# Performance work log

Hardware: AMD Instinct MI355X
Metric: run time of the kernel (lower is better)

## Reference

```python
import jax, jax.numpy as jnp
import numpy as np

N_NODES = 100_000
N_EDGES = 1_250_000
IN_FEATS, N_HIDDEN, N_CLASSES = 64, 64, 32


def setup_inputs() -> dict:
    key = jax.random.key(0)
    ks = jax.random.split(key, 8)
    x = jax.random.normal(ks[0], (N_NODES, IN_FEATS), dtype=jnp.float32)
    src = jax.random.randint(ks[1], (N_EDGES,), 0, N_NODES, dtype=jnp.int64)
    dst = jax.random.randint(ks[2], (N_EDGES,), 0, N_NODES, dtype=jnp.int64)
    s1 = 1.0 / np.sqrt(IN_FEATS)
    s2 = 1.0 / np.sqrt(N_HIDDEN)
    W_self1 = jax.random.normal(ks[3], (IN_FEATS, N_HIDDEN), dtype=jnp.float32) * s1
    W_neigh1 = jax.random.normal(ks[4], (IN_FEATS, N_HIDDEN), dtype=jnp.float32) * s1
    b1 = jnp.zeros((N_HIDDEN,), dtype=jnp.float32)
    W_self2 = jax.random.normal(ks[5], (N_HIDDEN, N_CLASSES), dtype=jnp.float32) * s2
    W_neigh2 = jax.random.normal(ks[6], (N_HIDDEN, N_CLASSES), dtype=jnp.float32) * s2
    b2 = jnp.zeros((N_CLASSES,), dtype=jnp.float32)
    return dict(x=x, src=src, dst=dst, W_self1=W_self1, W_neigh1=W_neigh1, b1=b1,
                W_self2=W_self2, W_neigh2=W_neigh2, b2=b2)


def _sage_conv(h, src, dst, W_self, W_neigh, b):
    # mean aggregation over in-neighbors: gather src feats, segment-sum by dst
    n = h.shape[0]
    msg = h[src]  # [E, d] -- dominant memory traffic
    agg = jax.ops.segment_sum(msg, dst, num_segments=n)
    deg = jax.ops.segment_sum(jnp.ones_like(dst, dtype=h.dtype), dst, num_segments=n)
    h_neigh = agg / jnp.maximum(deg, 1.0)[:, None]  # zero-degree nodes get 0 (DGL behavior)
    return h @ W_self + h_neigh @ W_neigh + b


def reference(x, src, dst, W_self1, W_neigh1, b1, W_self2, W_neigh2, b2):
    h = _sage_conv(x, src, dst, W_self1, W_neigh1, b1)
    h = jax.nn.relu(h)
    # dropout(p=0.5) is identity in eval mode
    return _sage_conv(h, src, dst, W_self2, W_neigh2, b2)
```

## Files before the change

### kernel.cpp

```cpp
#include <hip/hip_runtime.h>
#include <hip/hip_bf16.h>


#define NF 64
#define BW 256
#define BSH 8
#define MAXB 512
#define CAPMAX 8192
#define P1_CHUNK 2048
#define H1S 68

typedef __attribute__((ext_vector_type(8))) short short8;
typedef __attribute__((ext_vector_type(8))) unsigned short ushort8v;
typedef __attribute__((ext_vector_type(4))) float floatx4;

__device__ __forceinline__ short bf16hi(float v) {
    __hip_bfloat16 h = __float2bfloat16(v);
    return *(short*)&h;
}
__device__ __forceinline__ float bf2f(short s) {
    __hip_bfloat16 h = *(__hip_bfloat16*)&s;
    return __bfloat162float(h);
}
__device__ __forceinline__ float bits2f(unsigned short u) {
    unsigned int x = ((unsigned int)u) << 16;
    union { unsigned int i; float f; } c; c.i = x; return c.f;
}


__global__ __launch_bounds__(512) void zero_kernel(int* __restrict__ g) {
    if (threadIdx.x < MAXB) g[threadIdx.x] = 0;
}


__global__ __launch_bounds__(256) void p1_dense1_kernel(
        const int* __restrict__ src, const int* __restrict__ dst,
        int* __restrict__ gcursor, unsigned* __restrict__ bucket,
        int E, int nbuckets, int dblocks,
        const float* __restrict__ X,
        const float* __restrict__ Wself,
        const float* __restrict__ Wneigh,
        const float* __restrict__ bias,
        float* __restrict__ outA,
        unsigned short* __restrict__ outB,
        int N,
        const float* __restrict__ Ws2,
        const float* __restrict__ Wn2,
        unsigned short* __restrict__ w2p,
        int wpackBlk) {
    __shared__ int smem_i[9216];
    const int tid = threadIdx.x;

    if ((int)blockIdx.x == wpackBlk) {
        for (int i = tid; i < 64 * 64; i += 256) {
            int n = i & 63, k = i >> 6;
            float v = (n < 32) ? Ws2[k * 32 + n] : Wn2[k * 32 + (n - 32)];
            short hv = bf16hi(v);
            w2p[n * 64 + k] = (unsigned short)hv;
            w2p[4096 + n * 64 + k] = (unsigned short)bf16hi(v - bf2f(hv));
        }
        return;
    }

    if ((int)blockIdx.x >= dblocks) {
        int* cnt   = smem_i;
        int* cbase = smem_i + MAXB;
        const int bid = blockIdx.x - dblocks;
        const int beg = bid * P1_CHUNK;
        const int end = min(E, beg + P1_CHUNK);
        for (int i = tid; i < nbuckets; i += 256) cnt[i] = 0;
        __syncthreads();
        for (int e = beg + tid; e < end; e += 256)
            atomicAdd(&cnt[dst[e] >> BSH], 1);
        __syncthreads();
        for (int i = tid; i < nbuckets; i += 256) {
            int c = cnt[i];
            cbase[i] = c ? atomicAdd(&gcursor[i], c) : 0;
            cnt[i] = 0;
        }
        __syncthreads();
        for (int e = beg + tid; e < end; e += 256) {
            int d = dst[e];
            int r = d >> BSH;
            int p = cbase[r] + atomicAdd(&cnt[r], 1);
            if (p < CAPMAX)
                bucket[(size_t)r * CAPMAX + p] = ((unsigned)src[e] << BSH) | (unsigned)(d & (BW - 1));
        }
        return;
    }

    constexpr int NT = 8, NSELF = 4, NO = 128, HALF = 64;
    unsigned short* wh = (unsigned short*)smem_i;
    unsigned short* wl = wh + NO * 72;
    for (int i = tid; i < NO * 64; i += 256) {
        int n = i & (NO - 1), k = i / NO;
        float v = (n < HALF) ? Wself[k * HALF + n] : Wneigh[k * HALF + (n - HALF)];
        short hv = bf16hi(v);
        wh[n * 72 + k] = (unsigned short)hv;
        wl[n * 72 + k] = (unsigned short)bf16hi(v - bf2f(hv));
    }

    const int lane = tid & 63;
    const int wid  = tid >> 6;
    const int m = lane & 15, quad = lane >> 4;
    const int rowblk = blockIdx.x * 128 + wid * 32;

    floatx4 acc[2][NT];
    #pragma unroll
    for (int rt = 0; rt < 2; ++rt)
        #pragma unroll
        for (int t = 0; t < NT; ++t) acc[rt][t] = (floatx4)(0.f);

    short8 ah[2][2], al[2][2];
    #pragma unroll
    for (int rt = 0; rt < 2; ++rt) {
        int r = rowblk + rt * 16 + m;
        if (r >= N) r = N - 1;
        const float* xp = X + (size_t)r * 64 + quad * 8;
        #pragma unroll
        for (int h = 0; h < 2; ++h) {
            floatx4 f0 = *(const floatx4*)(xp + h * 32);
            floatx4 f1 = *(const floatx4*)(xp + h * 32 + 4);
            short8 hi, lo;
            #pragma unroll
            for (int j = 0; j < 4; ++j) {
                short hv = bf16hi(f0[j]);
                hi[j] = hv; lo[j] = bf16hi(f0[j] - bf2f(hv));
                short hv2 = bf16hi(f1[j]);
                hi[4 + j] = hv2; lo[4 + j] = bf16hi(f1[j] - bf2f(hv2));
            }
            ah[rt][h] = hi; al[rt][h] = lo;
        }
    }
    __syncthreads();

    #pragma unroll
    for (int t = 0; t < NT; ++t) {
        int n = t * 16 + m;
        const unsigned short* ph = wh + n * 72 + quad * 8;
        const unsigned short* pl = wl + n * 72 + quad * 8;
        #pragma unroll
        for (int h = 0; h < 2; ++h) {
            short8 bh = *(const short8*)(ph + h * 32);
            short8 bl = *(const short8*)(pl + h * 32);
            #pragma unroll
            for (int rt = 0; rt < 2; ++rt) {
                acc[rt][t] = __builtin_amdgcn_mfma_f32_16x16x32_bf16(ah[rt][h], bh, acc[rt][t], 0, 0, 0);
                acc[rt][t] = __builtin_amdgcn_mfma_f32_16x16x32_bf16(al[rt][h], bh, acc[rt][t], 0, 0, 0);
                acc[rt][t] = __builtin_amdgcn_mfma_f32_16x16x32_bf16(ah[rt][h], bl, acc[rt][t], 0, 0, 0);
            }
        }
    }

    #pragma unroll
    for (int rt = 0; rt < 2; ++rt) {
        #pragma unroll
        for (int t = 0; t < NT; ++t) {
            #pragma unroll
            for (int r4 = 0; r4 < 4; ++r4) {
                int row = rowblk + rt * 16 + quad * 4 + r4;
                if (row < N) {
                    if (t < NSELF) {
                        int col = t * 16 + m;
                        outA[(size_t)row * 64 + col] = acc[rt][t][r4] + bias[col];
                    } else {
                        int col = (t - NSELF) * 16 + m;
                        outB[(size_t)row * 64 + col] = (unsigned short)bf16hi(acc[rt][t][r4]);
                    }
                }
            }
        }
    }
}


__global__ __launch_bounds__(256) void p2_csr_kernel(const unsigned* __restrict__ bucket,
                                                     const int* __restrict__ gcursor,
                                                     int* __restrict__ row_start,
                                                     int* __restrict__ csr_src,
                                                     int N, int nbuckets) {
    __shared__ unsigned stage[CAPMAX];
    __shared__ int cnt[BW];
    __shared__ int excl[BW];
    const int r = blockIdx.x;
    const int tid = threadIdx.x;

    int partial = 0;
    for (int i = tid; i < r; i += 256) partial += min(gcursor[i], CAPMAX);
    excl[tid] = partial;
    __syncthreads();
    for (int off = 128; off > 0; off >>= 1) {
        if (tid < off) excl[tid] += excl[tid + off];
        __syncthreads();
    }
    const int base = excl[0];
    const int sz = min(gcursor[r], CAPMAX);
    const unsigned* bsrc = bucket + (size_t)r * CAPMAX;
    __syncthreads();

    cnt[tid] = 0;
    __syncthreads();
    for (int i = tid; i < sz; i += 256) {
        unsigned v = bsrc[i];
        stage[i] = v;
        atomicAdd(&cnt[v & (BW - 1)], 1);
    }
    __syncthreads();
    excl[tid] = cnt[tid];
    __syncthreads();
    for (int off = 1; off < BW; off <<= 1) {
        int v0 = (tid >= off) ? excl[tid - off] : 0;
        __syncthreads();
        excl[tid] += v0;
        __syncthreads();
    }
    int node = r * BW + tid;
    if (node < N) row_start[node] = base + excl[tid] - cnt[tid];
    if (r == nbuckets - 1 && tid == 0) row_start[N] = base + sz;
    __syncthreads();
    cnt[tid] = excl[tid] - cnt[tid];
    __syncthreads();
    for (int i = tid; i < sz; i += 256) {
        unsigned v = stage[i];
        int p = atomicAdd(&cnt[v & (BW - 1)], 1);
        csr_src[base + p] = (int)(v >> BSH);
    }
}


__global__ __launch_bounds__(256) void agg64_d2_kernel(
        const unsigned short* __restrict__ t1n,
        const float* __restrict__ xs,
        const int* __restrict__ row_start,
        const int* __restrict__ csr_src,
        const unsigned short* __restrict__ w2p,
        const float* __restrict__ b2,
        float* __restrict__ outD,
        unsigned short* __restrict__ t2n,
        int N) {
    __shared__ float h1s[16][H1S];
    const int tid = threadIdx.x;

    const int lane = tid & 63;
    const int wid  = tid >> 6;
    const int half = lane >> 5;
    const int g = (lane >> 3) & 3;
    const int c = lane & 7;
    const int nbase = blockIdx.x * 16;

    const int m = lane & 15, quad = lane >> 4;
    const int coln = wid * 16 + m;
    const unsigned short* pb = w2p + coln * 64 + quad * 8;
    short8 bhf[2], blf[2];
    #pragma unroll
    for (int h = 0; h < 2; ++h) {
        bhf[h] = *(const short8*)(pb + h * 32);
        blf[h] = *(const short8*)(pb + h * 32 + 4096);
    }

    #pragma unroll
    for (int q = 0; q < 2; ++q) {
        const int ln = wid * 4 + q * 2 + half;
        const int n = nbase + ln;
        float acc[8] = {0.f, 0.f, 0.f, 0.f, 0.f, 0.f, 0.f, 0.f};
        int beg = 0, end = 0;
        if (n < N) { beg = row_start[n]; end = row_start[n + 1]; }
        for (int j = beg + g; j < end; j += 8) {
            int j2 = j + 4;
            int s0 = csr_src[j];
            ushort8v u0 = *(const ushort8v*)(t1n + (size_t)s0 * 64 + c * 8);
            if (j2 < end) {
                int s1 = csr_src[j2];
                ushort8v u1 = *(const ushort8v*)(t1n + (size_t)s1 * 64 + c * 8);
                #pragma unroll
                for (int i = 0; i < 8; ++i) acc[i] += bits2f(u0[i]) + bits2f(u1[i]);
            } else {
                #pragma unroll
                for (int i = 0; i < 8; ++i) acc[i] += bits2f(u0[i]);
            }
        }
        #pragma unroll
        for (int i = 0; i < 8; ++i) {
            float v = acc[i];
            v += __shfl_xor(v, 8);
            v += __shfl_xor(v, 16);
            acc[i] = v;
        }
        if (g == 0) {
            floatx4 h0, h1v;
            if (n < N) {
                float invd = 1.0f / fmaxf((float)(end - beg), 1.0f);
                size_t o = (size_t)n * 64 + c * 8;
                floatx4 x0 = *(const floatx4*)(xs + o);
                floatx4 x1 = *(const floatx4*)(xs + o + 4);
                #pragma unroll
                for (int i = 0; i < 4; ++i) {
                    h0[i]  = fmaxf(x0[i] + acc[i] * invd, 0.f);
                    h1v[i] = fmaxf(x1[i] + acc[4 + i] * invd, 0.f);
                }
            } else {
                h0 = (floatx4)(0.f); h1v = (floatx4)(0.f);
            }
            *(floatx4*)&h1s[ln][c * 8]     = h0;
            *(floatx4*)&h1s[ln][c * 8 + 4] = h1v;
        }
    }
    __syncthreads();

    short8 ah[2], al[2];
    #pragma unroll
    for (int h = 0; h < 2; ++h) {
        const float* hp = &h1s[m][quad * 8 + h * 32];
        floatx4 f0 = *(const floatx4*)hp;
        floatx4 f1 = *(const floatx4*)(hp + 4);
        short8 hi, lo;
        #pragma unroll
        for (int j = 0; j < 4; ++j) {
            short hv = bf16hi(f0[j]);
            hi[j] = hv; lo[j] = bf16hi(f0[j] - bf2f(hv));
            short hv2 = bf16hi(f1[j]);
            hi[4 + j] = hv2; lo[4 + j] = bf16hi(f1[j] - bf2f(hv2));
        }
        ah[h] = hi; al[h] = lo;
    }
    floatx4 acc2 = (floatx4)(0.f);
    #pragma unroll
    for (int h = 0; h < 2; ++h) {
        acc2 = __builtin_amdgcn_mfma_f32_16x16x32_bf16(ah[h], bhf[h], acc2, 0, 0, 0);
        acc2 = __builtin_amdgcn_mfma_f32_16x16x32_bf16(al[h], bhf[h], acc2, 0, 0, 0);
        acc2 = __builtin_amdgcn_mfma_f32_16x16x32_bf16(ah[h], blf[h], acc2, 0, 0, 0);
    }
    #pragma unroll
    for (int r4 = 0; r4 < 4; ++r4) {
        int node = nbase + quad * 4 + r4;
        if (node < N) {
            if (coln < 32) outD[(size_t)node * 32 + coln] = acc2[r4] + b2[coln];
            else t2n[(size_t)node * 32 + (coln - 32)] = (unsigned short)bf16hi(acc2[r4]);
        }
    }
}


__global__ __launch_bounds__(256) void agg32_kernel(float* io,
                                                    const unsigned short* __restrict__ t2n,
                                                    const int* __restrict__ row_start,
                                                    const int* __restrict__ csr_src, int N) {
    int n = (blockIdx.x * blockDim.x + threadIdx.x) >> 6;
    if (n >= N) return;
    int lane = threadIdx.x & 63;
    int g = lane >> 2, c = lane & 3;
    int beg = row_start[n], end = row_start[n + 1];
    float acc[8] = {0.f, 0.f, 0.f, 0.f, 0.f, 0.f, 0.f, 0.f};
    for (int j = beg + g; j < end; j += 32) {
        int j2 = j + 16;
        int s0 = csr_src[j];
        ushort8v u0 = *(const ushort8v*)(t2n + (size_t)s0 * 32 + c * 8);
        if (j2 < end) {
            int s1 = csr_src[j2];
            ushort8v u1 = *(const ushort8v*)(t2n + (size_t)s1 * 32 + c * 8);
            #pragma unroll
            for (int i = 0; i < 8; ++i) acc[i] += bits2f(u0[i]) + bits2f(u1[i]);
        } else {
            #pragma unroll
            for (int i = 0; i < 8; ++i) acc[i] += bits2f(u0[i]);
        }
    }
    #pragma unroll
    for (int i = 0; i < 8; ++i) {
        float v = acc[i];
        v += __shfl_xor(v, 4);
        v += __shfl_xor(v, 8);
        v += __shfl_xor(v, 16);
        v += __shfl_xor(v, 32);
        acc[i] = v;
    }
    if (g == 0) {
        float inv = 1.0f / fmaxf((float)(end - beg), 1.0f);
        size_t o = (size_t)n * 32 + c * 8;
        floatx4 s0 = *(const floatx4*)(io + o);
        floatx4 s1 = *(const floatx4*)(io + o + 4);
        floatx4 r0, r1;
        #pragma unroll
        for (int i = 0; i < 4; ++i) {
            r0[i] = s0[i] + acc[i] * inv;
            r1[i] = s1[i] + acc[4 + i] * inv;
        }
        *(floatx4*)(io + o) = r0;
        *(floatx4*)(io + o + 4) = r1;
    }
}


__global__ __launch_bounds__(256) void deg_kernel(const int* __restrict__ dst,
                                                  float* __restrict__ deg, int E) {
    int e = blockIdx.x * blockDim.x + threadIdx.x;
    if (e < E) atomicAdd(&deg[dst[e]], 1.0f);
}

__global__ __launch_bounds__(256) void agg_atomic_kernel(const float* __restrict__ feats,
                                                         const int* __restrict__ src,
                                                         const int* __restrict__ dst,
                                                         float* __restrict__ agg, int E) {
    int tid = blockIdx.x * blockDim.x + threadIdx.x;
    if (tid >= E * NF) return;
    int e = tid >> 6, f = tid & 63;
    atomicAdd(&agg[(size_t)dst[e] * NF + f], feats[(size_t)src[e] * NF + f]);
}

__global__ __launch_bounds__(256) void layer1_fb_kernel(const float* __restrict__ x,
                                                        const float* __restrict__ agg,
                                                        const float* __restrict__ deg,
                                                        const float* __restrict__ Wself,
                                                        const float* __restrict__ Wneigh,
                                                        const float* __restrict__ b,
                                                        float* __restrict__ h1, int N) {
    int tid = blockIdx.x * blockDim.x + threadIdx.x;
    if (tid >= N * NF) return;
    int n = tid >> 6, c = tid & 63;
    float inv = 1.0f / fmaxf(deg[n], 1.0f);
    const float* xrow = x + (size_t)n * NF;
    const float* arow = agg + (size_t)n * NF;
    float acc = b[c];
    #pragma unroll
    for (int k = 0; k < NF; ++k) {
        acc += xrow[k] * Wself[k * NF + c];
        acc += (arow[k] * inv) * Wneigh[k * NF + c];
    }
    h1[tid] = fmaxf(acc, 0.f);
}

__global__ __launch_bounds__(256) void layer2_fb_kernel(const float* __restrict__ h1,
                                                        const float* __restrict__ agg,
                                                        const float* __restrict__ deg,
                                                        const float* __restrict__ Wself,
                                                        const float* __restrict__ Wneigh,
                                                        const float* __restrict__ b,
                                                        float* __restrict__ out, int N) {
    int tid = blockIdx.x * blockDim.x + threadIdx.x;
    if (tid >= N * 32) return;
    int n = tid >> 5, c = tid & 31;
    float inv = 1.0f / fmaxf(deg[n], 1.0f);
    const float* hrow = h1 + (size_t)n * NF;
    const float* arow = agg + (size_t)n * NF;
    float acc = b[c];
    #pragma unroll
    for (int k = 0; k < NF; ++k) {
        acc += hrow[k] * Wself[k * 32 + c];
        acc += (arow[k] * inv) * Wneigh[k * 32 + c];
    }
    out[tid] = acc;
}


extern "C" void kernel_launch(void* const* d_in, const int* in_sizes, int n_in,
                              void* d_out, int out_size, void* d_ws, size_t ws_size,
                              hipStream_t stream) {
    const float* x        = (const float*)d_in[0];
    const int*   src      = (const int*)d_in[1];
    const int*   dst      = (const int*)d_in[2];
    const float* W_self1  = (const float*)d_in[3];
    const float* W_neigh1 = (const float*)d_in[4];
    const float* b1       = (const float*)d_in[5];
    const float* W_self2  = (const float*)d_in[6];
    const float* W_neigh2 = (const float*)d_in[7];
    const float* b2       = (const float*)d_in[8];
    float* out = (float*)d_out;

    const int N = in_sizes[0] / NF;
    const int E = in_sizes[1];
    const int nbuckets = (N + BW - 1) / BW;

    const size_t rsPad = ((size_t)N + 8) & ~7ull;
    int* gcursor   = (int*)d_ws;
    unsigned short* w2p = (unsigned short*)(gcursor + MAXB);
    int* row_start = (int*)(w2p + 8192);
    int* csr_src   = row_start + rsPad;
    uintptr_t pa = (uintptr_t)(csr_src + (((size_t)E + 7) & ~7ull));
    pa = (pa + 127) & ~(uintptr_t)127;
    float* bufA = (float*)pa;
    unsigned* bucket = (unsigned*)bufA;
    unsigned short* t1n = (unsigned short*)(bufA + (size_t)N * NF);
    unsigned short* t2n = t1n + (size_t)N * NF;
    size_t need = (size_t)((char*)(t2n + (size_t)N * 32) - (char*)d_ws);

    bool fast = ws_size >= need
             && nbuckets <= MAXB
             && (size_t)nbuckets * CAPMAX <= (size_t)N * NF
             && (size_t)E * 2 / (size_t)nbuckets <= CAPMAX
             && N < (1 << 24)
             && out_size >= N * 32;

    if (fast) {
        zero_kernel<<<1, 512, 0, stream>>>(gcursor);
        int dblocks  = (N + 127) / 128;
        int p1blocks = (E + P1_CHUNK - 1) / P1_CHUNK;
        unsigned* bucket2 = (unsigned*)(t2n + (((size_t)N * 32 + 63) & ~63ull));
        size_t need2 = (size_t)((char*)(bucket2 + (size_t)nbuckets * CAPMAX) - (char*)d_ws);
        if (ws_size >= need2) {
            p1_dense1_kernel<<<dblocks + p1blocks + 1, 256, 0, stream>>>(
                src, dst, gcursor, bucket2, E, nbuckets, dblocks,
                x, W_self1, W_neigh1, b1, bufA, t1n, N,
                W_self2, W_neigh2, w2p, dblocks + p1blocks);
            p2_csr_kernel<<<nbuckets, 256, 0, stream>>>(bucket2, gcursor,
                                                        row_start, csr_src, N, nbuckets);
        } else {
            p1_dense1_kernel<<<p1blocks + 1, 256, 0, stream>>>(
                src, dst, gcursor, bucket, E, nbuckets, 0,
                x, W_self1, W_neigh1, b1, bufA, t1n, N,
                W_self2, W_neigh2, w2p, p1blocks);
            p2_csr_kernel<<<nbuckets, 256, 0, stream>>>(bucket, gcursor,
                                                        row_start, csr_src, N, nbuckets);
            p1_dense1_kernel<<<dblocks, 256, 0, stream>>>(
                src, dst, gcursor, bucket, E, nbuckets, dblocks,
                x, W_self1, W_neigh1, b1, bufA, t1n, N,
                W_self2, W_neigh2, w2p, -1);
        }
        agg64_d2_kernel<<<(N + 15) / 16, 256, 0, stream>>>(
            t1n, bufA, row_start, csr_src, w2p, b2, out, t2n, N);
        agg32_kernel<<<(N * 64 + 255) / 256, 256, 0, stream>>>(out, t2n,
                                                               row_start, csr_src, N);
    } else {
        float* deg = (float*)d_ws;
        float* agg = deg + N;
        float* h1  = agg + (size_t)N * NF;
        hipMemsetAsync(deg, 0, (size_t)(N + (size_t)N * NF) * sizeof(float), stream);
        deg_kernel<<<(E + 255) / 256, 256, 0, stream>>>(dst, deg, E);
        int at = E * NF;
        agg_atomic_kernel<<<(at + 255) / 256, 256, 0, stream>>>(x, src, dst, agg, E);
        layer1_fb_kernel<<<(N * NF + 255) / 256, 256, 0, stream>>>(x, agg, deg, W_self1,
                                                                   W_neigh1, b1, h1, N);
        hipMemsetAsync(agg, 0, (size_t)N * NF * sizeof(float), stream);
        agg_atomic_kernel<<<(at + 255) / 256, 256, 0, stream>>>(h1, src, dst, agg, E);
        layer2_fb_kernel<<<(N * 32 + 255) / 256, 256, 0, stream>>>(h1, agg, deg, W_self2,
                                                                   W_neigh2, b2, out, N);
    }
}
```

Baseline: 216.7 us.

## Prepack layer weights in a prep kernel and interleave two-node gathers in aggregation

Layer-1 and layer-2 weights are now split into hi/lo bf16 and packed once by a small prep kernel that also zeroes the cursors. The dense layer-1 blocks read the packed weights from global memory, so each block no longer repacks them into 36KB of LDS and waits on a barrier, which should also raise occupancy. The layer-2 aggregation walks both of a wave's nodes in one loop with four independent gathers in flight, using clamped indices and predicated adds. The self-feature loads are issued before the reduction to hide their latency. The cost is extra wasted loads when the two nodes differ in degree, and one more small launch.

```diff
diff --git a/kernel.cpp b/kernel.cpp
--- a/kernel.cpp
+++ b/kernel.cpp
@@ -28,8 +28,31 @@
 }
 
 
-__global__ __launch_bounds__(512) void zero_kernel(int* __restrict__ g) {
-    if (threadIdx.x < MAXB) g[threadIdx.x] = 0;
+__global__ __launch_bounds__(256) void prep_kernel(
+        int* __restrict__ gcursor,
+        const float* __restrict__ Ws1, const float* __restrict__ Wn1,
+        const float* __restrict__ Ws2, const float* __restrict__ Wn2,
+        unsigned short* __restrict__ w1p, unsigned short* __restrict__ w2p) {
+    const int tid = threadIdx.x;
+    if (blockIdx.x == 0) {
+        for (int i = tid; i < MAXB; i += 256) gcursor[i] = 0;
+        return;
+    }
+    const int part = blockIdx.x - 1;
+    for (int i = tid; i < 32 * 64; i += 256) {
+        int n = part * 32 + (i >> 6), k = i & 63;
+        float v = (n < 64) ? Ws1[k * 64 + n] : Wn1[k * 64 + (n - 64)];
+        short hv = bf16hi(v);
+        w1p[n * 64 + k] = (unsigned short)hv;
+        w1p[8192 + n * 64 + k] = (unsigned short)bf16hi(v - bf2f(hv));
+    }
+    for (int i = tid; i < 16 * 64; i += 256) {
+        int n = part * 16 + (i >> 6), k = i & 63;
+        float v = (n < 32) ? Ws2[k * 32 + n] : Wn2[k * 32 + (n - 32)];
+        short hv = bf16hi(v);
+        w2p[n * 64 + k] = (unsigned short)hv;
+        w2p[4096 + n * 64 + k] = (unsigned short)bf16hi(v - bf2f(hv));
+    }
 }
 
 
@@ -38,29 +61,13 @@
         int* __restrict__ gcursor, unsigned* __restrict__ bucket,
         int E, int nbuckets, int dblocks,
         const float* __restrict__ X,
-        const float* __restrict__ Wself,
-        const float* __restrict__ Wneigh,
+        const unsigned short* __restrict__ w1p,
         const float* __restrict__ bias,
         float* __restrict__ outA,
         unsigned short* __restrict__ outB,
-        int N,
-        const float* __restrict__ Ws2,
-        const float* __restrict__ Wn2,
-        unsigned short* __restrict__ w2p,
-        int wpackBlk) {
-    __shared__ int smem_i[9216];
+        int N) {
+    __shared__ int smem_i[2 * MAXB];
     const int tid = threadIdx.x;
-
-    if ((int)blockIdx.x == wpackBlk) {
-        for (int i = tid; i < 64 * 64; i += 256) {
-            int n = i & 63, k = i >> 6;
-            float v = (n < 32) ? Ws2[k * 32 + n] : Wn2[k * 32 + (n - 32)];
-            short hv = bf16hi(v);
-            w2p[n * 64 + k] = (unsigned short)hv;
-            w2p[4096 + n * 64 + k] = (unsigned short)bf16hi(v - bf2f(hv));
-        }
-        return;
-    }
 
     if ((int)blockIdx.x >= dblocks) {
         int* cnt   = smem_i;
@@ -89,17 +96,7 @@
         return;
     }
 
-    constexpr int NT = 8, NSELF = 4, NO = 128, HALF = 64;
-    unsigned short* wh = (unsigned short*)smem_i;
-    unsigned short* wl = wh + NO * 72;
-    for (int i = tid; i < NO * 64; i += 256) {
-        int n = i & (NO - 1), k = i / NO;
-        float v = (n < HALF) ? Wself[k * HALF + n] : Wneigh[k * HALF + (n - HALF)];
-        short hv = bf16hi(v);
-        wh[n * 72 + k] = (unsigned short)hv;
-        wl[n * 72 + k] = (unsigned short)bf16hi(v - bf2f(hv));
-    }
-
+    constexpr int NT = 8, NSELF = 4;
     const int lane = tid & 63;
     const int wid  = tid >> 6;
     const int m = lane & 15, quad = lane >> 4;
@@ -132,13 +129,12 @@
             ah[rt][h] = hi; al[rt][h] = lo;
         }
     }
-    __syncthreads();
 
     #pragma unroll
     for (int t = 0; t < NT; ++t) {
         int n = t * 16 + m;
-        const unsigned short* ph = wh + n * 72 + quad * 8;
-        const unsigned short* pl = wl + n * 72 + quad * 8;
+        const unsigned short* ph = w1p + n * 64 + quad * 8;
+        const unsigned short* pl = ph + 8192;
         #pragma unroll
         for (int h = 0; h < 2; ++h) {
             short8 bh = *(const short8*)(ph + h * 32);
@@ -237,10 +233,9 @@
         const float* __restrict__ b2,
         float* __restrict__ outD,
         unsigned short* __restrict__ t2n,
-        int N) {
+        int N, int E) {
     __shared__ float h1s[16][H1S];
     const int tid = threadIdx.x;
-
     const int lane = tid & 63;
     const int wid  = tid >> 6;
     const int half = lane >> 5;
@@ -248,62 +243,94 @@
     const int c = lane & 7;
     const int nbase = blockIdx.x * 16;
 
+    const int ln0 = wid * 4 + half;
+    const int ln1 = ln0 + 2;
+    const int n0 = nbase + ln0, n1 = nbase + ln1;
+    int beg0 = 0, end0 = 0, beg1 = 0, end1 = 0;
+    if (n0 < N) { beg0 = row_start[n0]; end0 = row_start[n0 + 1]; }
+    if (n1 < N) { beg1 = row_start[n1]; end1 = row_start[n1 + 1]; }
+
+    float a0[8] = {0.f, 0.f, 0.f, 0.f, 0.f, 0.f, 0.f, 0.f};
+    float a1[8] = {0.f, 0.f, 0.f, 0.f, 0.f, 0.f, 0.f, 0.f};
+    int j0 = beg0 + g, j1 = beg1 + g;
+    const int Em1 = E - 1;
+    while ((j0 < end0) || (j1 < end1)) {
+        int s0 = csr_src[min(j0, Em1)];
+        int s1 = csr_src[min(j0 + 4, Em1)];
+        int s2 = csr_src[min(j1, Em1)];
+        int s3 = csr_src[min(j1 + 4, Em1)];
+        s0 = ((unsigned)s0 < (unsigned)N) ? s0 : 0;
+        s1 = ((unsigned)s1 < (unsigned)N) ? s1 : 0;
+        s2 = ((unsigned)s2 < (unsigned)N) ? s2 : 0;
+        s3 = ((unsigned)s3 < (unsigned)N) ? s3 : 0;
+        ushort8v u0 = *(const ushort8v*)(t1n + (size_t)s0 * 64 + c * 8);
+        ushort8v u1 = *(const ushort8v*)(t1n + (size_t)s1 * 64 + c * 8);
+        ushort8v u2 = *(const ushort8v*)(t1n + (size_t)s2 * 64 + c * 8);
+        ushort8v u3 = *(const ushort8v*)(t1n + (size_t)s3 * 64 + c * 8);
+        const bool c00 = j0 < end0, c01 = j0 + 4 < end0;
+        const bool c10 = j1 < end1, c11 = j1 + 4 < end1;
+        #pragma unroll
+        for (int i = 0; i < 8; ++i) {
+            a0[i] += (c00 ? bits2f(u0[i]) : 0.f) + (c01 ? bits2f(u1[i]) : 0.f);
+            a1[i] += (c10 ? bits2f(u2[i]) : 0.f) + (c11 ? bits2f(u3[i]) : 0.f);
+        }
+        j0 += 8; j1 += 8;
+    }
+
     const int m = lane & 15, quad = lane >> 4;
     const int coln = wid * 16 + m;
     const unsigned short* pb = w2p + coln * 64 + quad * 8;
-    short8 bhf[2], blf[2];
-    #pragma unroll
-    for (int h = 0; h < 2; ++h) {
-        bhf[h] = *(const short8*)(pb + h * 32);
-        blf[h] = *(const short8*)(pb + h * 32 + 4096);
-    }
-
-    #pragma unroll
-    for (int q = 0; q < 2; ++q) {
-        const int ln = wid * 4 + q * 2 + half;
-        const int n = nbase + ln;
-        float acc[8] = {0.f, 0.f, 0.f, 0.f, 0.f, 0.f, 0.f, 0.f};
-        int beg = 0, end = 0;
-        if (n < N) { beg = row_start[n]; end = row_start[n + 1]; }
-        for (int j = beg + g; j < end; j += 8) {
-            int j2 = j + 4;
-            int s0 = csr_src[j];
-            ushort8v u0 = *(const ushort8v*)(t1n + (size_t)s0 * 64 + c * 8);
-            if (j2 < end) {
-                int s1 = csr_src[j2];
-                ushort8v u1 = *(const ushort8v*)(t1n + (size_t)s1 * 64 + c * 8);
-                #pragma unroll
-                for (int i = 0; i < 8; ++i) acc[i] += bits2f(u0[i]) + bits2f(u1[i]);
-            } else {
-                #pragma unroll
-                for (int i = 0; i < 8; ++i) acc[i] += bits2f(u0[i]);
+    short8 bhf0 = *(const short8*)(pb);
+    short8 bhf1 = *(const short8*)(pb + 32);
+    short8 blf0 = *(const short8*)(pb + 4096);
+    short8 blf1 = *(const short8*)(pb + 4096 + 32);
+
+    floatx4 x00 = (floatx4)(0.f), x01 = (floatx4)(0.f);
+    floatx4 x10 = (floatx4)(0.f), x11 = (floatx4)(0.f);
+    if (g == 0) {
+        if (n0 < N) {
+            const float* p = xs + (size_t)n0 * 64 + c * 8;
+            x00 = *(const floatx4*)p; x01 = *(const floatx4*)(p + 4);
+        }
+        if (n1 < N) {
+            const float* p = xs + (size_t)n1 * 64 + c * 8;
+            x10 = *(const floatx4*)p; x11 = *(const floatx4*)(p + 4);
+        }
+    }
+
+    #pragma unroll
+    for (int i = 0; i < 8; ++i) {
+        float v = a0[i];
+        v += __shfl_xor(v, 8);
+        v += __shfl_xor(v, 16);
+        a0[i] = v;
+        float w = a1[i];
+        w += __shfl_xor(w, 8);
+        w += __shfl_xor(w, 16);
+        a1[i] = w;
+    }
+    if (g == 0) {
+        floatx4 h0, h1v;
+        if (n0 < N) {
+            float invd = 1.0f / fmaxf((float)(end0 - beg0), 1.0f);
+            #pragma unroll
+            for (int i = 0; i < 4; ++i) {
+                h0[i]  = fmaxf(x00[i] + a0[i] * invd, 0.f);
+                h1v[i] = fmaxf(x01[i] + a0[4 + i] * invd, 0.f);
             }
-        }
-        #pragma unroll
-        for (int i = 0; i < 8; ++i) {
-            float v = acc[i];
-            v += __shfl_xor(v, 8);
-            v += __shfl_xor(v, 16);
-            acc[i] = v;
-        }
-        if (g == 0) {
-            floatx4 h0, h1v;
-            if (n < N) {
-                float invd = 1.0f / fmaxf((float)(end - beg), 1.0f);
-                size_t o = (size_t)n * 64 + c * 8;
-                floatx4 x0 = *(const floatx4*)(xs + o);
-                floatx4 x1 = *(const floatx4*)(xs + o + 4);
-                #pragma unroll
-                for (int i = 0; i < 4; ++i) {
-                    h0[i]  = fmaxf(x0[i] + acc[i] * invd, 0.f);
-                    h1v[i] = fmaxf(x1[i] + acc[4 + i] * invd, 0.f);
-                }
-            } else {
-                h0 = (floatx4)(0.f); h1v = (floatx4)(0.f);
+        } else { h0 = (floatx4)(0.f); h1v = (floatx4)(0.f); }
+        *(floatx4*)&h1s[ln0][c * 8]     = h0;
+        *(floatx4*)&h1s[ln0][c * 8 + 4] = h1v;
+        if (n1 < N) {
+            float invd = 1.0f / fmaxf((float)(end1 - beg1), 1.0f);
+            #pragma unroll
+            for (int i = 0; i < 4; ++i) {
+                h0[i]  = fmaxf(x10[i] + a1[i] * invd, 0.f);
+                h1v[i] = fmaxf(x11[i] + a1[4 + i] * invd, 0.f);
             }
-            *(floatx4*)&h1s[ln][c * 8]     = h0;
-            *(floatx4*)&h1s[ln][c * 8 + 4] = h1v;
-        }
+        } else { h0 = (floatx4)(0.f); h1v = (floatx4)(0.f); }
+        *(floatx4*)&h1s[ln1][c * 8]     = h0;
+        *(floatx4*)&h1s[ln1][c * 8 + 4] = h1v;
     }
     __syncthreads();
 
@@ -324,12 +351,12 @@
         ah[h] = hi; al[h] = lo;
     }
     floatx4 acc2 = (floatx4)(0.f);
-    #pragma unroll
-    for (int h = 0; h < 2; ++h) {
-        acc2 = __builtin_amdgcn_mfma_f32_16x16x32_bf16(ah[h], bhf[h], acc2, 0, 0, 0);
-        acc2 = __builtin_amdgcn_mfma_f32_16x16x32_bf16(al[h], bhf[h], acc2, 0, 0, 0);
-        acc2 = __builtin_amdgcn_mfma_f32_16x16x32_bf16(ah[h], blf[h], acc2, 0, 0, 0);
-    }
+    acc2 = __builtin_amdgcn_mfma_f32_16x16x32_bf16(ah[0], bhf0, acc2, 0, 0, 0);
+    acc2 = __builtin_amdgcn_mfma_f32_16x16x32_bf16(al[0], bhf0, acc2, 0, 0, 0);
+    acc2 = __builtin_amdgcn_mfma_f32_16x16x32_bf16(ah[0], blf0, acc2, 0, 0, 0);
+    acc2 = __builtin_amdgcn_mfma_f32_16x16x32_bf16(ah[1], bhf1, acc2, 0, 0, 0);
+    acc2 = __builtin_amdgcn_mfma_f32_16x16x32_bf16(al[1], bhf1, acc2, 0, 0, 0);
+    acc2 = __builtin_amdgcn_mfma_f32_16x16x32_bf16(ah[1], blf1, acc2, 0, 0, 0);
     #pragma unroll
     for (int r4 = 0; r4 < 4; ++r4) {
         int node = nbase + quad * 4 + r4;
@@ -350,6 +377,12 @@
     int lane = threadIdx.x & 63;
     int g = lane >> 2, c = lane & 3;
     int beg = row_start[n], end = row_start[n + 1];
+    floatx4 s0v = (floatx4)(0.f), s1v = (floatx4)(0.f);
+    size_t o = (size_t)n * 32 + c * 8;
+    if (g == 0) {
+        s0v = *(const floatx4*)(io + o);
+        s1v = *(const floatx4*)(io + o + 4);
+    }
     float acc[8] = {0.f, 0.f, 0.f, 0.f, 0.f, 0.f, 0.f, 0.f};
     for (int j = beg + g; j < end; j += 32) {
         int j2 = j + 16;
@@ -376,14 +409,11 @@
     }
     if (g == 0) {
         float inv = 1.0f / fmaxf((float)(end - beg), 1.0f);
-        size_t o = (size_t)n * 32 + c * 8;
-        floatx4 s0 = *(const floatx4*)(io + o);
-        floatx4 s1 = *(const floatx4*)(io + o + 4);
         floatx4 r0, r1;
         #pragma unroll
         for (int i = 0; i < 4; ++i) {
-            r0[i] = s0[i] + acc[i] * inv;
-            r1[i] = s1[i] + acc[4 + i] * inv;
+            r0[i] = s0v[i] + acc[i] * inv;
+            r1[i] = s1v[i] + acc[4 + i] * inv;
         }
         *(floatx4*)(io + o) = r0;
         *(floatx4*)(io + o + 4) = r1;
@@ -473,7 +503,8 @@
     const size_t rsPad = ((size_t)N + 8) & ~7ull;
     int* gcursor   = (int*)d_ws;
     unsigned short* w2p = (unsigned short*)(gcursor + MAXB);
-    int* row_start = (int*)(w2p + 8192);
+    unsigned short* w1p = w2p + 8192;
+    int* row_start = (int*)(w1p + 16384);
     int* csr_src   = row_start + rsPad;
     uintptr_t pa = (uintptr_t)(csr_src + (((size_t)E + 7) & ~7ull));
     pa = (pa + 127) & ~(uintptr_t)127;
@@ -491,32 +522,30 @@
              && out_size >= N * 32;
 
     if (fast) {
-        zero_kernel<<<1, 512, 0, stream>>>(gcursor);
+        prep_kernel<<<5, 256, 0, stream>>>(gcursor, W_self1, W_neigh1,
+                                           W_self2, W_neigh2, w1p, w2p);
         int dblocks  = (N + 127) / 128;
         int p1blocks = (E + P1_CHUNK - 1) / P1_CHUNK;
         unsigned* bucket2 = (unsigned*)(t2n + (((size_t)N * 32 + 63) & ~63ull));
         size_t need2 = (size_t)((char*)(bucket2 + (size_t)nbuckets * CAPMAX) - (char*)d_ws);
         if (ws_size >= need2) {
-            p1_dense1_kernel<<<dblocks + p1blocks + 1, 256, 0, stream>>>(
+            p1_dense1_kernel<<<dblocks + p1blocks, 256, 0, stream>>>(
                 src, dst, gcursor, bucket2, E, nbuckets, dblocks,
-                x, W_self1, W_neigh1, b1, bufA, t1n, N,
-                W_self2, W_neigh2, w2p, dblocks + p1blocks);
+                x, w1p, b1, bufA, t1n, N);
             p2_csr_kernel<<<nbuckets, 256, 0, stream>>>(bucket2, gcursor,
                                                         row_start, csr_src, N, nbuckets);
         } else {
-            p1_dense1_kernel<<<p1blocks + 1, 256, 0, stream>>>(
+            p1_dense1_kernel<<<p1blocks, 256, 0, stream>>>(
                 src, dst, gcursor, bucket, E, nbuckets, 0,
-                x, W_self1, W_neigh1, b1, bufA, t1n, N,
-                W_self2, W_neigh2, w2p, p1blocks);
+                x, w1p, b1, bufA, t1n, N);
             p2_csr_kernel<<<nbuckets, 256, 0, stream>>>(bucket, gcursor,
                                                         row_start, csr_src, N, nbuckets);
             p1_dense1_kernel<<<dblocks, 256, 0, stream>>>(
                 src, dst, gcursor, bucket, E, nbuckets, dblocks,
-                x, W_self1, W_neigh1, b1, bufA, t1n, N,
-                W_self2, W_neigh2, w2p, -1);
+                x, w1p, b1, bufA, t1n, N);
         }
         agg64_d2_kernel<<<(N + 15) / 16, 256, 0, stream>>>(
-            t1n, bufA, row_start, csr_src, w2p, b2, out, t2n, N);
+            t1n, bufA, row_start, csr_src, w2p, b2, out, t2n, N, E);
         agg32_kernel<<<(N * 64 + 255) / 256, 256, 0, stream>>>(out, t2n,
                                                                row_start, csr_src, N);
     } else {
```

After: 213.8 us. No clear change (-1.3%).
